# Kernel tuning notes

Measured on AMD Instinct MI355X. Metric: run time of the kernel, lower is better.

The kernel has to match this reference:

```python
import jax, jax.numpy as jnp
import numpy as np

B, NB, NA, D, PF = 16384, 8, 16, 128, 1
IN_DIM = D + NA * D + D  # basis + flattened sf + task = 2304
QK_DIM = D * 3 * PF      # 384
V_DIM = D * PF           # 128


def rbf_similarity(x, y):
    # RBF kernel over the feature axis: exp(-0.5 * ||x - y||^2)
    return jnp.exp(-0.5 * jnp.sum((x - y) ** 2, axis=-1))


def setup_inputs() -> dict:
    key = jax.random.key(0)
    ks = jax.random.split(key, 9)
    basis = jax.random.normal(ks[0], (B, NB, D), dtype=jnp.float32)
    sf_all = jax.random.normal(ks[1], (B, NB, NA, D), dtype=jnp.float32)
    task = jax.random.normal(ks[2], (B, NB, D), dtype=jnp.float32)
    mask = (jax.random.uniform(ks[3], (B, NB, D * PF)) > 0.5).astype(jnp.float32)
    s_in = 1.0 / np.sqrt(IN_DIM)
    s_v = 1.0 / np.sqrt(D)
    Wq = jax.random.normal(ks[4], (IN_DIM, QK_DIM), dtype=jnp.float32) * s_in
    Wk = jax.random.normal(ks[5], (IN_DIM, QK_DIM), dtype=jnp.float32) * s_in
    bk = jnp.zeros((QK_DIM,), dtype=jnp.float32)
    Wv = jax.random.normal(ks[6], (D, V_DIM), dtype=jnp.float32) * s_v
    bv = jnp.zeros((V_DIM,), dtype=jnp.float32)
    return {"basis_features_all": basis, "sf_all": sf_all, "task": task, "mask": mask,
            "Wq": Wq, "Wk": Wk, "bk": bk, "Wv": Wv, "bv": bv}


def reference(basis_features_all, sf_all, task, mask, Wq, Wk, bk, Wv, bv):
    b = sf_all.shape[0]
    sf_all_r = jnp.reshape(sf_all, (b, NB, NA * D))          # (B, NB, NA*D)
    sf_first_r = sf_all_r[:, :1, :]                          # (B, 1, NA*D)
    task = jax.lax.stop_gradient(task)
    task_n = task / jnp.linalg.norm(task, ord=2, axis=-1, keepdims=True)

    # RBF similarity side-branch between consecutive beakers
    bst = jnp.concatenate([basis_features_all, sf_all_r, task_n], axis=-1)  # (B, NB, IN_DIM)
    sim = rbf_similarity(bst[:, :-1, :], bst[:, 1:, :]).mean(axis=0)        # (NB-1,)

    bf_first = basis_features_all[:, :1, :]
    bf_rest = jax.lax.stop_gradient(basis_features_all[:, 1:, :])
    bf_all = jnp.concatenate([bf_first, bf_rest], axis=1)

    q_in = jnp.concatenate([bf_first, sf_first_r, task_n[:, :1, :]], axis=-1)  # (B, 1, IN_DIM)
    query = q_in @ Wq                                                          # (B, 1, QK)
    k_in = jnp.concatenate([bf_all, sf_all_r, task_n], axis=-1)                # (B, NB, IN_DIM)
    keys = k_in @ Wk + bk                                                      # (B, NB, QK)
    values = sf_all @ Wv + bv                                                  # (B, NB, NA, V)

    mask_rep = jnp.repeat(mask, 3, axis=-1)                                    # (B, NB, QK)
    keys_masked = keys * mask_rep
    values_masked = values

    attn_logits = jnp.matmul(query, jnp.swapaxes(keys_masked, -2, -1)) / jnp.sqrt(jnp.float32(D * PF))
    attn_logits = jnp.where(attn_logits == 0, -1e9, attn_logits)               # zero-mask trick
    attention_weights = jax.nn.softmax(attn_logits, axis=-1)                   # (B, 1, NB)

    attended_sf = jnp.einsum('bna,baqf->bnqf', attention_weights, values_masked)  # (B, 1, NA, V)
    task_first = task[:, 0, :]                                                    # (B, D)
    q_1 = jnp.einsum('bi,bnji->bj', task_first, attended_sf)                      # (B, NA)
    return (q_1, attended_sf, attn_logits, attention_weights, keys_masked, values_masked, sim)
```

## Files before the change

### kernel.cpp

```cpp
#include <hip/hip_runtime.h>
#include <hip/hip_bf16.h>
#include <math.h>

static constexpr size_t OFF_ATT = 262144;
static constexpr size_t OFF_LOG = 33816576;
static constexpr size_t OFF_W   = 33947648;
static constexpr size_t OFF_KM  = 34078720;
static constexpr size_t OFF_VM  = 84410368;
static constexpr size_t OFF_SIM = 352845824;

typedef short bf16x8 __attribute__((ext_vector_type(8)));
typedef float f32x4 __attribute__((ext_vector_type(4)));

__device__ inline unsigned short f2bf(float f) {
  union { float f; unsigned u; } x; x.f = f;
  unsigned r = x.u + 0x7FFFu + ((x.u >> 16) & 1u);
  return (unsigned short)(r >> 16);
}

__device__ inline float wave_sum(float v) {
#pragma unroll
  for (int o = 32; o > 0; o >>= 1) v += __shfl_xor(v, o, 64);
  return v;
}

__global__ void norm_kernel(const float* __restrict__ task, float* __restrict__ invn,
                            float* __restrict__ simo) {
  int idx = blockIdx.x * 4 + (threadIdx.x >> 6);
  int lane = threadIdx.x & 63;
  float t0 = task[(size_t)idx * 128 + lane];
  float t1 = task[(size_t)idx * 128 + 64 + lane];
  float s = wave_sum(t0 * t0 + t1 * t1);
  if (lane == 0) invn[idx] = rsqrtf(s);
  if (blockIdx.x == 0 && threadIdx.x < 7) simo[threadIdx.x] = 0.0f;
}

__global__ void wprep_t(const float* __restrict__ W, unsigned short* __restrict__ WT,
                        int K, int N) {
  int ntn = N >> 6;
  int kt = blockIdx.x / ntn, nt = blockIdx.x % ntn;
  int k0 = kt * 64, n0 = nt * 64;
  __shared__ float t[64][65];
  int tid = threadIdx.x;
  int r = tid >> 2, c0 = (tid & 3) * 16;
#pragma unroll
  for (int q = 0; q < 4; ++q) {
    float4 v = *(const float4*)(W + (size_t)(k0 + r) * N + n0 + c0 + q * 4);
    t[r][c0 + q * 4 + 0] = v.x; t[r][c0 + q * 4 + 1] = v.y;
    t[r][c0 + q * 4 + 2] = v.z; t[r][c0 + q * 4 + 3] = v.w;
  }
  __syncthreads();
  int n = tid >> 2, kc0 = (tid & 3) * 16;
#pragma unroll
  for (int q = 0; q < 4; ++q) {
    int kc = kc0 + q * 4;
    ushort4 o = make_ushort4(f2bf(t[kc + 0][n]), f2bf(t[kc + 1][n]),
                             f2bf(t[kc + 2][n]), f2bf(t[kc + 3][n]));
    *(ushort4*)(WT + (size_t)(n0 + n) * K + k0 + kc) = o;
  }
}

__global__ __launch_bounds__(576) void abuild_sim(const float* __restrict__ basis,
                                                  const float* __restrict__ sf,
                                                  const float* __restrict__ task,
                                                  const float* __restrict__ invn,
                                                  unsigned short* __restrict__ Abf,
                                                  float* __restrict__ simo) {
  int b = blockIdx.x;
  int f = threadIdx.x;
  size_t row0 = (size_t)b * 8;
  float4 v[8];
#pragma unroll
  for (int n = 0; n < 8; ++n) {
    size_t row = row0 + n;
    float4 x;
    if (f < 32)       x = *(const float4*)(basis + row * 128 + f * 4);
    else if (f < 544) x = *(const float4*)(sf + row * 2048 + (f - 32) * 4);
    else {
      x = *(const float4*)(task + row * 128 + (f - 544) * 4);
      float s = invn[row];
      x.x *= s; x.y *= s; x.z *= s; x.w *= s;
    }
    v[n] = x;
    ushort4 o = make_ushort4(f2bf(x.x), f2bf(x.y), f2bf(x.z), f2bf(x.w));
    *(ushort4*)(Abf + row * 2304 + f * 4) = o;
  }
  float s7[7];
#pragma unroll
  for (int n = 1; n < 8; ++n) {
    float dx = v[n].x - v[n - 1].x, dy = v[n].y - v[n - 1].y;
    float dz = v[n].z - v[n - 1].z, dw = v[n].w - v[n - 1].w;
    s7[n - 1] = dx * dx + dy * dy + dz * dz + dw * dw;
  }
  __shared__ float red[9][7];
  int wid = threadIdx.x >> 6, lane = threadIdx.x & 63;
#pragma unroll
  for (int i = 0; i < 7; ++i) {
    float p = wave_sum(s7[i]);
    if (lane == 0) red[wid][i] = p;
  }
  __syncthreads();
  if (threadIdx.x < 7) {
    float s = 0.f;
#pragma unroll
    for (int w = 0; w < 9; ++w) s += red[w][threadIdx.x];
    atomicAdd(&simo[threadIdx.x], expf(-0.5f * s) * (1.0f / 16384.0f));
  }
}

__global__ __launch_bounds__(256) void qk2(const unsigned short* __restrict__ Abf,
                                           const unsigned short* __restrict__ WkT,
                                           const unsigned short* __restrict__ WqT,
                                           const float* __restrict__ bias,
                                           const float* __restrict__ mask,
                                           float* __restrict__ km,
                                           float* __restrict__ query) {
  __shared__ unsigned short As[2 * 4096];
  __shared__ unsigned short Bs[2 * 4096];
  int bid = blockIdx.x;
  bool isq = bid >= 3072;
  int mt, nt;
  const unsigned short* WT;
  float* outp;
  if (!isq) {
    int swz = (bid & 7) * 384 + (bid >> 3);
    mt = swz / 3; nt = swz - mt * 3;
    WT = WkT; outp = km;
  } else {
    int q = bid - 3072;
    int swz = (q & 7) * 48 + (q >> 3);
    mt = swz / 3; nt = swz - mt * 3;
    WT = WqT; outp = query;
  }
  int tid = threadIdx.x;
  int wave = tid >> 6, lane = tid & 63;
  int wr = wave >> 1, wc = wave & 1;
  int m0g = mt * 128, n0g = nt * 128;

  int c_lo = wave * 128 + lane;
  int row_q0 = c_lo >> 2, kc_q0 = ((c_lo & 3) ^ ((row_q0 >> 1) & 3)) * 8;
  int c_hi = c_lo + 64;
  int row_q1 = c_hi >> 2, kc_q1 = ((c_hi & 3) ^ ((row_q1 >> 1) & 3)) * 8;
  size_t ga_q0 = isq ? (size_t)(m0g + row_q0) * 8 : (size_t)(m0g + row_q0);
  size_t ga_q1 = isq ? (size_t)(m0g + row_q1) * 8 : (size_t)(m0g + row_q1);
  const unsigned short* ag0 = Abf + ga_q0 * 2304 + kc_q0;
  const unsigned short* ag1 = Abf + ga_q1 * 2304 + kc_q1;
  const unsigned short* bg0 = WT + (size_t)(n0g + row_q0) * 2304 + kc_q0;
  const unsigned short* bg1 = WT + (size_t)(n0g + row_q1) * 2304 + kc_q1;
  int ldsoff0 = wave * 1024;
  int ldsoff1 = ldsoff0 + 512;

#define STAGE(ks, cur)                                                                   \
  do {                                                                                   \
    int _k0 = (ks) * 32;                                                                 \
    unsigned short* _a = As + (cur) * 4096;                                              \
    unsigned short* _b = Bs + (cur) * 4096;                                              \
    __builtin_amdgcn_global_load_lds(                                                    \
        (const __attribute__((address_space(1))) void*)(ag0 + _k0),                      \
        (__attribute__((address_space(3))) void*)(_a + ldsoff0), 16, 0, 0);              \
    __builtin_amdgcn_global_load_lds(                                                    \
        (const __attribute__((address_space(1))) void*)(ag1 + _k0),                      \
        (__attribute__((address_space(3))) void*)(_a + ldsoff1), 16, 0, 0);              \
    __builtin_amdgcn_global_load_lds(                                                    \
        (const __attribute__((address_space(1))) void*)(bg0 + _k0),                      \
        (__attribute__((address_space(3))) void*)(_b + ldsoff0), 16, 0, 0);              \
    __builtin_amdgcn_global_load_lds(                                                    \
        (const __attribute__((address_space(1))) void*)(bg1 + _k0),                      \
        (__attribute__((address_space(3))) void*)(_b + ldsoff1), 16, 0, 0);              \
  } while (0)

  f32x4 acc[4][4];
#pragma unroll
  for (int i = 0; i < 4; ++i)
#pragma unroll
    for (int j = 0; j < 4; ++j) acc[i][j] = (f32x4)(0.f);

  int la = lane & 15;
  int sl = (((lane >> 4) ^ ((la >> 1) & 3))) * 8;

  STAGE(0, 0);
  __syncthreads();
  int cur = 0;
  for (int ks = 0; ks < 72; ++ks) {
    if (ks < 71) STAGE(ks + 1, cur ^ 1);
    const unsigned short* aL = As + cur * 4096;
    const unsigned short* bL = Bs + cur * 4096;
    bf16x8 af[4], bf[4];
#pragma unroll
    for (int mi = 0; mi < 4; ++mi)
      af[mi] = *(const bf16x8*)(aL + (wr * 64 + mi * 16 + la) * 32 + sl);
#pragma unroll
    for (int ni = 0; ni < 4; ++ni)
      bf[ni] = *(const bf16x8*)(bL + (wc * 64 + ni * 16 + la) * 32 + sl);
#pragma unroll
    for (int mi = 0; mi < 4; ++mi)
#pragma unroll
      for (int ni = 0; ni < 4; ++ni)
        acc[mi][ni] = __builtin_amdgcn_mfma_f32_16x16x32_bf16(af[mi], bf[ni], acc[mi][ni], 0, 0, 0);
    __syncthreads();
    cur ^= 1;
  }
#undef STAGE

  int rq = lane >> 4;
#pragma unroll
  for (int mi = 0; mi < 4; ++mi) {
#pragma unroll
    for (int ni = 0; ni < 4; ++ni) {
      int colg = nt * 128 + wc * 64 + ni * 16 + la;
#pragma unroll
      for (int j = 0; j < 4; ++j) {
        int rowg = mt * 128 + wr * 64 + mi * 16 + rq * 4 + j;
        float v = acc[mi][ni][j];
        if (!isq)
          v = (v + bias[colg]) * mask[(size_t)rowg * 128 + (unsigned)colg / 3u];
        outp[(size_t)rowg * 384 + colg] = v;
      }
    }
  }
}

__global__ __launch_bounds__(256) void attn_kernel4(const float* __restrict__ query,
                                                    const float* __restrict__ km,
                                                    float* __restrict__ logits,
                                                    float* __restrict__ wts) {
  int w = threadIdx.x >> 6, lane = threadIdx.x & 63;
  int b = blockIdx.x * 4 + w;
  float q[6];
#pragma unroll
  for (int j = 0; j < 6; ++j) q[j] = query[(size_t)b * 384 + lane + 64 * j];
  float lg[8];
#pragma unroll
  for (int n = 0; n < 8; ++n) {
    const float* kr = km + ((size_t)b * 8 + n) * 384;
    float p = 0.f;
#pragma unroll
    for (int j = 0; j < 6; ++j) p = fmaf(q[j], kr[lane + 64 * j], p);
    p = wave_sum(p);
    float l = p * 0.08838834764831845f;
    lg[n] = (l == 0.0f) ? -1e9f : l;
  }
  float m = lg[0];
#pragma unroll
  for (int i = 1; i < 8; ++i) m = fmaxf(m, lg[i]);
  float ex[8], s = 0.f;
#pragma unroll
  for (int i = 0; i < 8; ++i) { ex[i] = expf(lg[i] - m); s += ex[i]; }
  float inv = 1.0f / s;
  if (lane < 8) {
    float lv = lg[0], ev = ex[0];
#pragma unroll
    for (int i = 1; i < 8; ++i)
      if (lane == i) { lv = lg[i]; ev = ex[i]; }
    logits[(size_t)b * 8 + lane] = lv;
    wts[(size_t)b * 8 + lane] = ev * inv;
  }
}

template <int ABF>
__global__ __launch_bounds__(256) void v_gemm_attend(const float* __restrict__ sf,
                                                     const unsigned short* __restrict__ Abf,
                                                     const float* __restrict__ Wv,
                                                     const unsigned short* __restrict__ WvT,
                                                     const float* __restrict__ bv,
                                                     const float* __restrict__ wts,
                                                     const float* __restrict__ task,
                                                     float* __restrict__ vm,
                                                     float* __restrict__ att,
                                                     float* __restrict__ q1) {
  __shared__ unsigned short As[2 * 4096];
  __shared__ unsigned short Bs[128 * 136];
  float* attL = (float*)As;
  int bid = blockIdx.x;
  int swz = (bid & 7) * 2048 + (bid >> 3);
  int b = swz;
  size_t m0 = (size_t)swz * 128;
  int tid = threadIdx.x;
  int wave = tid >> 6, lane = tid & 63;
  int wr = wave >> 1, wc = wave & 1;
  int r = tid >> 1, h = tid & 1;
  int la = lane & 15, lkq = lane >> 4;
  int sl = ((lkq ^ ((la >> 1) & 3))) * 8;

  if (ABF) {
#pragma unroll
    for (int q = 0; q < 8; ++q) {
      bf16x8 v = *(const bf16x8*)(WvT + (size_t)r * 128 + h * 64 + q * 8);
      *(bf16x8*)(Bs + r * 136 + h * 64 + q * 8) = v;
    }
  } else {
#pragma unroll
    for (int q = 0; q < 16; ++q) {
      int flat = q * 256 + tid;
      int k = flat >> 5;
      int n4 = (flat & 31) * 4;
      float4 v = *(const float4*)(Wv + (size_t)k * 128 + n4);
      Bs[(n4 + 0) * 136 + k] = f2bf(v.x);
      Bs[(n4 + 1) * 136 + k] = f2bf(v.y);
      Bs[(n4 + 2) * 136 + k] = f2bf(v.z);
      Bs[(n4 + 3) * 136 + k] = f2bf(v.w);
    }
  }

  const unsigned short *ap0 = nullptr, *ap1 = nullptr;
  int ldsA0 = wave * 1024, ldsA1 = ldsA0 + 512;
  if (ABF) {
    int p0 = wave * 128 + lane;
    int tr0 = p0 >> 2, ds0 = (p0 & 3) ^ ((tr0 >> 1) & 3);
    int p1 = p0 + 64;
    int tr1 = p1 >> 2, ds1 = (p1 & 3) ^ ((tr1 >> 1) & 3);
    ap0 = Abf + ((size_t)b * 8 + (tr0 >> 4)) * 2304 + 128 + (tr0 & 15) * 128 + ds0 * 8;
    ap1 = Abf + ((size_t)b * 8 + (tr1 >> 4)) * 2304 + 128 + (tr1 & 15) * 128 + ds1 * 8;
    __builtin_amdgcn_global_load_lds(
        (const __attribute__((address_space(1))) void*)(ap0),
        (__attribute__((address_space(3))) void*)(As + ldsA0), 16, 0, 0);
    __builtin_amdgcn_global_load_lds(
        (const __attribute__((address_space(1))) void*)(ap1),
        (__attribute__((address_space(3))) void*)(As + ldsA1), 16, 0, 0);
  }

  f32x4 acc[4][4];
#pragma unroll
  for (int i = 0; i < 4; ++i)
#pragma unroll
    for (int j = 0; j < 4; ++j) acc[i][j] = (f32x4)(0.f);

  if (ABF) __syncthreads();

  int cur = 0;
  for (int ks = 0; ks < 4; ++ks) {
    int k0 = ks * 32;
    if (ABF) {
      if (ks < 3) {
        __builtin_amdgcn_global_load_lds(
            (const __attribute__((address_space(1))) void*)(ap0 + k0 + 32),
            (__attribute__((address_space(3))) void*)(As + (cur ^ 1) * 4096 + ldsA0), 16, 0, 0);
        __builtin_amdgcn_global_load_lds(
            (const __attribute__((address_space(1))) void*)(ap1 + k0 + 32),
            (__attribute__((address_space(3))) void*)(As + (cur ^ 1) * 4096 + ldsA1), 16, 0, 0);
      }
    } else {
      const float* ap = sf + (m0 + r) * 128 + k0 + h * 16;
      float4 v0 = *(const float4*)(ap);
      float4 v1 = *(const float4*)(ap + 4);
      float4 v2 = *(const float4*)(ap + 8);
      float4 v3 = *(const float4*)(ap + 12);
      ushort4 p0 = make_ushort4(f2bf(v0.x), f2bf(v0.y), f2bf(v0.z), f2bf(v0.w));
      ushort4 p1 = make_ushort4(f2bf(v1.x), f2bf(v1.y), f2bf(v1.z), f2bf(v1.w));
      ushort4 p2 = make_ushort4(f2bf(v2.x), f2bf(v2.y), f2bf(v2.z), f2bf(v2.w));
      ushort4 p3 = make_ushort4(f2bf(v3.x), f2bf(v3.y), f2bf(v3.z), f2bf(v3.w));
      *(ushort4*)(As + r * 40 + h * 16)      = p0;
      *(ushort4*)(As + r * 40 + h * 16 + 4)  = p1;
      *(ushort4*)(As + r * 40 + h * 16 + 8)  = p2;
      *(ushort4*)(As + r * 40 + h * 16 + 12) = p3;
      __syncthreads();
    }
    const unsigned short* aL = ABF ? (As + cur * 4096) : As;
    bf16x8 af[4], bfr[4];
#pragma unroll
    for (int mi = 0; mi < 4; ++mi) {
      int rowl = wr * 64 + mi * 16 + la;
      af[mi] = ABF ? *(const bf16x8*)(aL + rowl * 32 + sl)
                   : *(const bf16x8*)(aL + rowl * 40 + lkq * 8);
    }
#pragma unroll
    for (int ni = 0; ni < 4; ++ni)
      bfr[ni] = *(const bf16x8*)(Bs + (wc * 64 + ni * 16 + la) * 136 + k0 + lkq * 8);
#pragma unroll
    for (int mi = 0; mi < 4; ++mi)
#pragma unroll
      for (int ni = 0; ni < 4; ++ni)
        acc[mi][ni] = __builtin_amdgcn_mfma_f32_16x16x32_bf16(af[mi], bfr[ni], acc[mi][ni], 0, 0, 0);
    __syncthreads();
    cur ^= 1;
  }

  float w4[4];
#pragma unroll
  for (int mi = 0; mi < 4; ++mi) w4[mi] = wts[(size_t)b * 8 + wr * 4 + mi];
  float pacc[4][4];
#pragma unroll
  for (int ni = 0; ni < 4; ++ni)
#pragma unroll
    for (int j = 0; j < 4; ++j) pacc[ni][j] = 0.f;
#pragma unroll
  for (int mi = 0; mi < 4; ++mi) {
#pragma unroll
    for (int ni = 0; ni < 4; ++ni) {
      int colg = wc * 64 + ni * 16 + la;
      float bb = bv[colg];
#pragma unroll
      for (int j = 0; j < 4; ++j) {
        size_t rowg = m0 + wr * 64 + mi * 16 + lkq * 4 + j;
        float v = acc[mi][ni][j] + bb;
        vm[rowg * 128 + colg] = v;
        pacc[ni][j] = fmaf(w4[mi], v, pacc[ni][j]);
      }
    }
  }
  if (wr == 0) {
#pragma unroll
    for (int ni = 0; ni < 4; ++ni)
#pragma unroll
      for (int j = 0; j < 4; ++j)
        attL[(lkq * 4 + j) * 132 + wc * 64 + ni * 16 + la] = pacc[ni][j];
  }
  __syncthreads();
  if (wr == 1) {
#pragma unroll
    for (int ni = 0; ni < 4; ++ni)
#pragma unroll
      for (int j = 0; j < 4; ++j)
        attL[(lkq * 4 + j) * 132 + wc * 64 + ni * 16 + la] += pacc[ni][j];
  }
  __syncthreads();
#pragma unroll
  for (int i = 0; i < 2; ++i) {
    int fidx = tid + i * 256;
    int a = fidx >> 5, c = (fidx & 31) * 4;
    f32x4 vv = *(const f32x4*)(attL + a * 132 + c);
    *(f32x4*)(att + (size_t)b * 2048 + a * 128 + c) = vv;
  }
  for (int j = wave; j < 16; j += 4) {
    float p = task[(size_t)b * 1024 + lane] * attL[j * 132 + lane]
            + task[(size_t)b * 1024 + 64 + lane] * attL[j * 132 + 64 + lane];
    p = wave_sum(p);
    if (lane == 0) q1[(size_t)b * 16 + j] = p;
  }
}

extern "C" void kernel_launch(void* const* d_in, const int* in_sizes, int n_in,
                              void* d_out, int out_size, void* d_ws, size_t ws_size,
                              hipStream_t stream) {
  const float* basis = (const float*)d_in[0];
  const float* sf    = (const float*)d_in[1];
  const float* task  = (const float*)d_in[2];
  const float* mask  = (const float*)d_in[3];
  const float* Wq    = (const float*)d_in[4];
  const float* Wk    = (const float*)d_in[5];
  const float* bk    = (const float*)d_in[6];
  const float* Wv    = (const float*)d_in[7];
  const float* bv    = (const float*)d_in[8];

  float* out  = (float*)d_out;
  float* q1   = out;
  float* att  = out + OFF_ATT;
  float* logi = out + OFF_LOG;
  float* wts  = out + OFF_W;
  float* km   = out + OFF_KM;
  float* vm   = out + OFF_VM;
  float* simo = out + OFF_SIM;

  constexpr size_t WS_NEED = 603979776ull + 1769472ull + 1769472ull + 32768ull +
                             25165824ull + 524288ull;
  bool usews = ws_size >= WS_NEED;

  unsigned short *Abf, *WkT, *WqT, *WvT = nullptr;
  float *query, *invn;
  if (usews) {
    unsigned char* ws = (unsigned char*)d_ws;
    Abf   = (unsigned short*)ws;
    WkT   = (unsigned short*)(ws + 603979776ull);
    WqT   = (unsigned short*)(ws + 605749248ull);
    WvT   = (unsigned short*)(ws + 607518720ull);
    query = (float*)(ws + 607551488ull);
    invn  = (float*)(ws + 632717312ull);
  } else {
    query = att;
    invn  = att + 6291456;
    WkT   = (unsigned short*)(att + 6422528);
    WqT   = WkT + 884736;
    Abf   = (unsigned short*)vm;
  }

  norm_kernel<<<32768, 256, 0, stream>>>(task, invn, simo);
  wprep_t<<<216, 256, 0, stream>>>(Wk, WkT, 2304, 384);
  wprep_t<<<216, 256, 0, stream>>>(Wq, WqT, 2304, 384);
  if (usews) wprep_t<<<4, 256, 0, stream>>>(Wv, WvT, 128, 128);
  abuild_sim<<<16384, 576, 0, stream>>>(basis, sf, task, invn, Abf, simo);
  qk2<<<3456, 256, 0, stream>>>(Abf, WkT, WqT, bk, mask, km, query);
  attn_kernel4<<<4096, 256, 0, stream>>>(query, km, logi, wts);
  if (usews)
    v_gemm_attend<1><<<16384, 256, 0, stream>>>(sf, Abf, Wv, WvT, bv, wts, task, vm, att, q1);
  else
    v_gemm_attend<0><<<16384, 256, 0, stream>>>(sf, nullptr, Wv, nullptr, bv, wts, task, vm, att, q1);
}
```

Before: 1.294 ms.

## Fuse norm into abuild, merge weight preps, fold attention softmax into V GEMM

The task-row normalization moves into the A-building kernel, where the last wave computes the norms with shuffles. This removes a separate pass over task and the invn buffer. The three weight-transpose launches become one launch, and the q·k logits and softmax are computed inside the V GEMM kernel instead of a separate attention kernel. This cuts kernel launches and global round-trips, at the cost of extra per-block work and a barrier at the start of the V GEMM.

```diff
diff --git a/kernel.cpp b/kernel.cpp
--- a/kernel.cpp
+++ b/kernel.cpp
@@ -35,6 +35,38 @@
   if (blockIdx.x == 0 && threadIdx.x < 7) simo[threadIdx.x] = 0.0f;
 }
 
+__global__ void wprep3(const float* __restrict__ Wk, const float* __restrict__ Wq,
+                       const float* __restrict__ Wv,
+                       unsigned short* __restrict__ WkT, unsigned short* __restrict__ WqT,
+                       unsigned short* __restrict__ WvT) {
+  int bb = blockIdx.x;
+  const float* W; unsigned short* WT; int K, N, b2;
+  if (bb < 216)      { W = Wk; WT = WkT; K = 2304; N = 384; b2 = bb; }
+  else if (bb < 432) { W = Wq; WT = WqT; K = 2304; N = 384; b2 = bb - 216; }
+  else               { W = Wv; WT = WvT; K = 128;  N = 128; b2 = bb - 432; }
+  int ntn = N >> 6;
+  int kt = b2 / ntn, nt = b2 % ntn;
+  int k0 = kt * 64, n0 = nt * 64;
+  __shared__ float t[64][65];
+  int tid = threadIdx.x;
+  int r = tid >> 2, c0 = (tid & 3) * 16;
+#pragma unroll
+  for (int q = 0; q < 4; ++q) {
+    float4 v = *(const float4*)(W + (size_t)(k0 + r) * N + n0 + c0 + q * 4);
+    t[r][c0 + q * 4 + 0] = v.x; t[r][c0 + q * 4 + 1] = v.y;
+    t[r][c0 + q * 4 + 2] = v.z; t[r][c0 + q * 4 + 3] = v.w;
+  }
+  __syncthreads();
+  int n = tid >> 2, kc0 = (tid & 3) * 16;
+#pragma unroll
+  for (int q = 0; q < 4; ++q) {
+    int kc = kc0 + q * 4;
+    ushort4 o = make_ushort4(f2bf(t[kc + 0][n]), f2bf(t[kc + 1][n]),
+                             f2bf(t[kc + 2][n]), f2bf(t[kc + 3][n]));
+    *(ushort4*)(WT + (size_t)(n0 + n) * K + k0 + kc) = o;
+  }
+}
+
 __global__ void wprep_t(const float* __restrict__ W, unsigned short* __restrict__ WT,
                         int K, int N) {
   int ntn = N >> 6;
@@ -57,6 +89,65 @@
     ushort4 o = make_ushort4(f2bf(t[kc + 0][n]), f2bf(t[kc + 1][n]),
                              f2bf(t[kc + 2][n]), f2bf(t[kc + 3][n]));
     *(ushort4*)(WT + (size_t)(n0 + n) * K + k0 + kc) = o;
+  }
+}
+
+__global__ __launch_bounds__(576) void abuild_sim_fn(const float* __restrict__ basis,
+                                                     const float* __restrict__ sf,
+                                                     const float* __restrict__ task,
+                                                     unsigned short* __restrict__ Abf,
+                                                     float* __restrict__ simo) {
+  int b = blockIdx.x;
+  int f = threadIdx.x;
+  size_t row0 = (size_t)b * 8;
+  float4 v[8];
+  if (f >= 544) {
+    float ss[8];
+#pragma unroll
+    for (int n = 0; n < 8; ++n) {
+      float4 x = *(const float4*)(task + (row0 + n) * 128 + (f - 544) * 4);
+      v[n] = x;
+      ss[n] = x.x * x.x + x.y * x.y + x.z * x.z + x.w * x.w;
+    }
+#pragma unroll
+    for (int n = 0; n < 8; ++n) {
+#pragma unroll
+      for (int o = 16; o > 0; o >>= 1) ss[n] += __shfl_xor(ss[n], o, 64);
+      float iv = rsqrtf(ss[n]);
+      v[n].x *= iv; v[n].y *= iv; v[n].z *= iv; v[n].w *= iv;
+    }
+  } else if (f < 32) {
+#pragma unroll
+    for (int n = 0; n < 8; ++n) v[n] = *(const float4*)(basis + (row0 + n) * 128 + f * 4);
+  } else {
+#pragma unroll
+    for (int n = 0; n < 8; ++n) v[n] = *(const float4*)(sf + (row0 + n) * 2048 + (f - 32) * 4);
+  }
+#pragma unroll
+  for (int n = 0; n < 8; ++n) {
+    ushort4 o = make_ushort4(f2bf(v[n].x), f2bf(v[n].y), f2bf(v[n].z), f2bf(v[n].w));
+    *(ushort4*)(Abf + (row0 + n) * 2304 + f * 4) = o;
+  }
+  float s7[7];
+#pragma unroll
+  for (int n = 1; n < 8; ++n) {
+    float dx = v[n].x - v[n - 1].x, dy = v[n].y - v[n - 1].y;
+    float dz = v[n].z - v[n - 1].z, dw = v[n].w - v[n - 1].w;
+    s7[n - 1] = dx * dx + dy * dy + dz * dz + dw * dw;
+  }
+  __shared__ float red[9][7];
+  int wid = threadIdx.x >> 6, lane = threadIdx.x & 63;
+#pragma unroll
+  for (int i = 0; i < 7; ++i) {
+    float p = wave_sum(s7[i]);
+    if (lane == 0) red[wid][i] = p;
+  }
+  __syncthreads();
+  if (threadIdx.x < 7) {
+    float s = 0.f;
+#pragma unroll
+    for (int w = 0; w < 9; ++w) s += red[w][threadIdx.x];
+    atomicAdd(&simo[threadIdx.x], expf(-0.5f * s) * (1.0f / 16384.0f));
   }
 }
 
@@ -257,7 +348,7 @@
   }
 }
 
-template <int ABF>
+template <int ABF, int FATTN>
 __global__ __launch_bounds__(256) void v_gemm_attend(const float* __restrict__ sf,
                                                      const unsigned short* __restrict__ Abf,
                                                      const float* __restrict__ Wv,
@@ -265,11 +356,17 @@
                                                      const float* __restrict__ bv,
                                                      const float* __restrict__ wts,
                                                      const float* __restrict__ task,
+                                                     const float* __restrict__ km,
+                                                     const float* __restrict__ query,
+                                                     float* __restrict__ logits,
+                                                     float* __restrict__ wtso,
                                                      float* __restrict__ vm,
                                                      float* __restrict__ att,
                                                      float* __restrict__ q1) {
   __shared__ unsigned short As[2 * 4096];
   __shared__ unsigned short Bs[128 * 136];
+  __shared__ float lgS[8];
+  __shared__ float wtsS[8];
   float* attL = (float*)As;
   int bid = blockIdx.x;
   int swz = (bid & 7) * 2048 + (bid >> 3);
@@ -319,13 +416,46 @@
         (__attribute__((address_space(3))) void*)(As + ldsA1), 16, 0, 0);
   }
 
+  if (FATTN) {
+    const float* qr = query + (size_t)b * 384;
+#pragma unroll
+    for (int i = 0; i < 2; ++i) {
+      int n = wave * 2 + i;
+      const float* kr = km + ((size_t)b * 8 + n) * 384;
+      float p = 0.f;
+#pragma unroll
+      for (int j = 0; j < 6; ++j) p = fmaf(qr[lane + 64 * j], kr[lane + 64 * j], p);
+      p = wave_sum(p);
+      if (lane == 0) {
+        float l = p * 0.08838834764831845f;
+        l = (l == 0.0f) ? -1e9f : l;
+        lgS[n] = l;
+        logits[(size_t)b * 8 + n] = l;
+      }
+    }
+  }
+
   f32x4 acc[4][4];
 #pragma unroll
   for (int i = 0; i < 4; ++i)
 #pragma unroll
     for (int j = 0; j < 4; ++j) acc[i][j] = (f32x4)(0.f);
 
-  if (ABF) __syncthreads();
+  if (ABF || FATTN) __syncthreads();
+
+  if (FATTN) {
+    if (tid < 8) {
+      float m = lgS[0];
+#pragma unroll
+      for (int i = 1; i < 8; ++i) m = fmaxf(m, lgS[i]);
+      float s = 0.f;
+#pragma unroll
+      for (int i = 0; i < 8; ++i) s += expf(lgS[i] - m);
+      float w = expf(lgS[tid] - m) / s;
+      wtsS[tid] = w;
+      wtso[(size_t)b * 8 + tid] = w;
+    }
+  }
 
   int cur = 0;
   for (int ks = 0; ks < 4; ++ks) {
@@ -377,7 +507,8 @@
 
   float w4[4];
 #pragma unroll
-  for (int mi = 0; mi < 4; ++mi) w4[mi] = wts[(size_t)b * 8 + wr * 4 + mi];
+  for (int mi = 0; mi < 4; ++mi)
+    w4[mi] = FATTN ? wtsS[wr * 4 + mi] : wts[(size_t)b * 8 + wr * 4 + mi];
   float pacc[4][4];
 #pragma unroll
   for (int ni = 0; ni < 4; ++ni)
@@ -465,23 +596,29 @@
     WvT   = (unsigned short*)(ws + 607518720ull);
     query = (float*)(ws + 607551488ull);
     invn  = (float*)(ws + 632717312ull);
+
+    hipMemsetAsync(simo, 0, 7 * sizeof(float), stream);
+    wprep3<<<436, 256, 0, stream>>>(Wk, Wq, Wv, WkT, WqT, WvT);
+    abuild_sim_fn<<<16384, 576, 0, stream>>>(basis, sf, task, Abf, simo);
+    qk2<<<3456, 256, 0, stream>>>(Abf, WkT, WqT, bk, mask, km, query);
+    v_gemm_attend<1, 1><<<16384, 256, 0, stream>>>(sf, Abf, Wv, WvT, bv, nullptr,
+                                                   task, km, query, logi, wts,
+                                                   vm, att, q1);
   } else {
     query = att;
     invn  = att + 6291456;
     WkT   = (unsigned short*)(att + 6422528);
     WqT   = WkT + 884736;
     Abf   = (unsigned short*)vm;
-  }
-
-  norm_kernel<<<32768, 256, 0, stream>>>(task, invn, simo);
-  wprep_t<<<216, 256, 0, stream>>>(Wk, WkT, 2304, 384);
-  wprep_t<<<216, 256, 0, stream>>>(Wq, WqT, 2304, 384);
-  if (usews) wprep_t<<<4, 256, 0, stream>>>(Wv, WvT, 128, 128);
-  abuild_sim<<<16384, 576, 0, stream>>>(basis, sf, task, invn, Abf, simo);
-  qk2<<<3456, 256, 0, stream>>>(Abf, WkT, WqT, bk, mask, km, query);
-  attn_kernel4<<<4096, 256, 0, stream>>>(query, km, logi, wts);
-  if (usews)
-    v_gemm_attend<1><<<16384, 256, 0, stream>>>(sf, Abf, Wv, WvT, bv, wts, task, vm, att, q1);
-  else
-    v_gemm_attend<0><<<16384, 256, 0, stream>>>(sf, nullptr, Wv, nullptr, bv, wts, task, vm, att, q1);
-}
+
+    norm_kernel<<<32768, 256, 0, stream>>>(task, invn, simo);
+    wprep_t<<<216, 256, 0, stream>>>(Wk, WkT, 2304, 384);
+    wprep_t<<<216, 256, 0, stream>>>(Wq, WqT, 2304, 384);
+    abuild_sim<<<16384, 576, 0, stream>>>(basis, sf, task, invn, Abf, simo);
+    qk2<<<3456, 256, 0, stream>>>(Abf, WkT, WqT, bk, mask, km, query);
+    attn_kernel4<<<4096, 256, 0, stream>>>(query, km, logi, wts);
+    v_gemm_attend<0, 0><<<16384, 256, 0, stream>>>(sf, nullptr, Wv, nullptr, bv, wts,
+                                                   task, nullptr, nullptr, nullptr,
+                                                   nullptr, vm, att, q1);
+  }
+}
```

After: 1.255 ms. -3.0%, faster.
